# Optimization experiments

Measured on AMD Instinct MI355X. Metric: run time of the kernel, lower is better.

Reference implementation:

```python
import jax, jax.numpy as jnp
import numpy as np

H = 16           # attn_num
ROPE_THETA = 10000.0

def _rope(x):
    # x: [B, H, S, A]; non-interleaved (rotate-half) RoPE matching RotaryEmb
    A = x.shape[-1]
    S = x.shape[2]
    inv_freq = (1.0 / ROPE_THETA) ** (jnp.arange(0, A, 2, dtype=jnp.float32) / A)  # [A/2]
    t = jnp.arange(S, dtype=jnp.float32)
    freqs = t[:, None] * inv_freq[None, :]            # [S, A/2]
    cos = jnp.cos(freqs)[None, None, :, :]
    sin = jnp.sin(freqs)[None, None, :, :]
    x1, x2 = jnp.split(x, 2, axis=-1)
    y1 = x1 * cos + x2 * sin
    y2 = -x1 * sin + x2 * cos
    return jnp.concatenate([y1, y2], axis=-1).astype(x.dtype)

def setup_inputs() -> dict:
    key = jax.random.key(0)
    kq, kk, kv = jax.random.split(key, 3)
    B, S, D = 2, 2048, 2048
    return {
        "xq": jax.random.normal(kq, (B, S, D), dtype=jnp.float32),
        "xk": jax.random.normal(kk, (B, S, D), dtype=jnp.float32),
        "xv": jax.random.normal(kv, (B, S, D), dtype=jnp.float32),
    }

def reference(xq, xk, xv):
    B, S, D = xq.shape
    A = D // H
    # b s (h a) -> b h s a
    q = xq.reshape(B, S, H, A).transpose(0, 2, 1, 3)
    k = xk.reshape(B, S, H, A).transpose(0, 2, 1, 3)
    v = xv.reshape(B, S, H, A).transpose(0, 2, 1, 3)
    q = _rope(q)
    k = _rope(k)
    scale = 1.0 / jnp.sqrt(jnp.asarray(A, dtype=q.dtype))
    scores = jnp.einsum('bhsa,bhta->bhst', q, k) * scale   # [B,H,S,S]
    causal = jnp.tril(jnp.ones((S, S), dtype=bool))
    scores = jnp.where(causal[None, None, :, :], scores, jnp.asarray(-jnp.inf, scores.dtype))
    probs = jax.nn.softmax(scores, axis=-1)
    out = jnp.einsum('bhst,bhta->bhsa', probs, v)          # [B,H,S,A]
    # b h s a -> b s (h a)
    return out.transpose(0, 2, 1, 3).reshape(B, S, D)
```

## Files before the change

### kernel.cpp

```cpp
#include <hip/hip_runtime.h>
#include <stdint.h>

#define H_HEADS 16
#define ADIM    128
#define SLEN    2048
#define DMODEL  2048

typedef __attribute__((ext_vector_type(8))) short  short8;
typedef __attribute__((ext_vector_type(4))) float  float4v;
typedef __attribute__((ext_vector_type(4))) unsigned short ushort4v;

typedef const __attribute__((address_space(1))) unsigned int gas_u32;
typedef __attribute__((address_space(3))) unsigned int las_u32;

union F4 { float4 v; float a[4]; };
union PU { unsigned u[4]; short8 s; };

__device__ __forceinline__ unsigned short f2bf(float f) {
  union { float f; unsigned u; } v; v.f = f;
  unsigned r = v.u + 0x7FFFu + ((v.u >> 16) & 1u);
  return (unsigned short)(r >> 16);
}

__device__ __forceinline__ unsigned cvt_pk_bf16(float lo, float hi) {
  unsigned r;
  asm("v_cvt_pk_bf16_f32 %0, %1, %2" : "=v"(r) : "v"(lo), "v"(hi));
  return r;
}

__device__ __forceinline__ void xswap(unsigned& a, unsigned& b) {
  asm volatile("v_permlane32_swap_b32 %0, %1" : "+v"(a), "+v"(b));
  asm volatile("v_permlane16_swap_b32 %0, %1" : "+v"(a), "+v"(b));
}

__device__ __forceinline__ float fsin01(float r) { float o; asm("v_sin_f32 %0, %1" : "=v"(o) : "v"(r)); return o; }
__device__ __forceinline__ float fcos01(float r) { float o; asm("v_cos_f32 %0, %1" : "=v"(o) : "v"(r)); return o; }
__device__ __forceinline__ float ffract(float x) { float o; asm("v_fract_f32 %0, %1" : "=v"(o) : "v"(x)); return o; }
__device__ __forceinline__ float hexp2(float x)  { float o; asm("v_exp_f32 %0, %1" : "=v"(o) : "v"(x)); return o; }

#define ROPE_C 0.20762050593045935f
#define L2I2PI -2.651496129472319f
#define C2LOG  0.12751879523103988f
#define Z0     8.0f

__global__ __launch_bounds__(256) void prep_k(const float* __restrict__ xk,
                                              unsigned short* __restrict__ kw) {
  int t = blockIdx.x * 256 + threadIdx.x;
  int i4 = t & 15;
  int h  = (t >> 4) & (H_HEADS - 1);
  int s  = (t >> 8) & (SLEN - 1);
  int b  = t >> 19;
  int i0 = i4 * 4;
  long ib = ((long)(b * SLEN + s)) * DMODEL + h * ADIM;
  F4 x1, x2;
  x1.v = *(const float4*)(xk + ib + i0);
  x2.v = *(const float4*)(xk + ib + i0 + 64);
  ushort4v o1, o2;
  #pragma unroll
  for (int j = 0; j < 4; ++j) {
    float rev = (float)s * exp2f(fmaf(-(float)(i0 + j), ROPE_C, L2I2PI));
    float r = ffract(rev);
    float sn = fsin01(r), cs = fcos01(r);
    o1[j] = f2bf( x1.a[j] * cs + x2.a[j] * sn);
    o2[j] = f2bf(-x1.a[j] * sn + x2.a[j] * cs);
  }
  long row = ((long)((b * H_HEADS + h) * SLEN + s)) * ADIM;
  int swz = s & 7;
  int c1 = ((((i0     ) >> 3) ^ swz) << 3) | (i0 & 7);
  int c2 = ((((i0 + 64) >> 3) ^ swz) << 3) | (i0 & 7);
  *(ushort4v*)(kw + row + c1) = o1;
  *(ushort4v*)(kw + row + c2) = o2;
}

__global__ __launch_bounds__(256) void prep_v(const float* __restrict__ xv,
                                              unsigned short* __restrict__ vw) {
  __shared__ float lv[64 * 129];
  int jt = blockIdx.x;
  int bh = blockIdx.y;
  int b = bh >> 4, h = bh & (H_HEADS - 1);
  int t = threadIdx.x;
  #pragma unroll
  for (int it = 0; it < 8; ++it) {
    int id  = it * 256 + t;
    int row = id >> 5;
    int c4  = (id & 31) * 4;
    F4 x;
    x.v = *(const float4*)(xv + ((long)(b * SLEN + jt * 64 + row)) * DMODEL + h * ADIM + c4);
    #pragma unroll
    for (int j = 0; j < 4; ++j) lv[row * 129 + c4 + j] = x.a[j];
  }
  __syncthreads();
  int l = t & 63, w = t >> 6;
  unsigned short* vt = vw + ((long)(bh * 32 + jt)) * 8192;
  #pragma unroll
  for (int it = 0; it < 8; ++it) {
    int d = it * 16 + w * 4 + (l >> 4);
    int i = l & 15;
    ushort4v o;
    #pragma unroll
    for (int j = 0; j < 4; ++j) o[j] = f2bf(lv[(4 * i + j) * 129 + d]);
    int off = d * 64 + ((((i >> 1) ^ (d & 7)) << 3) | ((i & 1) << 2));
    *(ushort4v*)(vt + off) = o;
  }
}

__global__ __launch_bounds__(512, 1) void attn_fwd(const float* __restrict__ xq,
                                                   const unsigned short* __restrict__ kw,
                                                   const unsigned short* __restrict__ vw,
                                                   float* __restrict__ out) {
  __shared__ __align__(16) unsigned short kL[2][2][64 * 128];
  __shared__ __align__(16) unsigned short vL[2][2][128 * 64];

  int n = blockIdx.x;
  int xcd = n & 7;
  int j   = (n < 256) ? (n >> 3) : ((n - 256) >> 3);
  int bh  = xcd * 4 + (j & 3);
  int c   = (n < 256) ? (15 - (j >> 2)) : (7 - (j >> 2));
  int b = bh >> 4, h = bh & (H_HEADS - 1);
  int t = threadIdx.x, l = t & 63, w = t >> 6;
  int g = w >> 2, ww = w & 3;
  int lq = l & 15, gq = l >> 4, lq7 = lq & 7;
  int basew = c * 128 + ww * 32;
  int sq0 = basew + lq, sq1 = basew + 16 + lq;

  short8 qf0[4], qf1[4];
  auto ROPEQ = [&](int sq, short8 (&qf)[4]) {
    const float* qsrc = xq + ((long)(b * SLEN + sq)) * DMODEL + h * ADIM;
    float q32[4][8];
    #pragma unroll
    for (int cc = 0; cc < 4; ++cc) {
      F4 lo, hi;
      lo.v = *(const float4*)(qsrc + cc * 32 + gq * 8);
      hi.v = *(const float4*)(qsrc + cc * 32 + gq * 8 + 4);
      #pragma unroll
      for (int jj = 0; jj < 4; ++jj) { q32[cc][jj] = lo.a[jj]; q32[cc][jj + 4] = hi.a[jj]; }
    }
    #pragma unroll
    for (int cc = 0; cc < 2; ++cc) {
      #pragma unroll
      for (int jj = 0; jj < 8; ++jj) {
        int a = cc * 32 + gq * 8 + jj;
        float rev = (float)sq * exp2f(fmaf(-(float)a, ROPE_C, L2I2PI));
        float r = ffract(rev);
        float sn = fsin01(r), cs = fcos01(r);
        qf[cc    ][jj] = (short)f2bf( q32[cc][jj] * cs + q32[cc + 2][jj] * sn);
        qf[cc + 2][jj] = (short)f2bf(-q32[cc][jj] * sn + q32[cc + 2][jj] * cs);
      }
    }
  };
  ROPEQ(sq0, qf0);
  ROPEQ(sq1, qf1);

  float4v acc0[8], acc1[8], lacc0, lacc1;
  #pragma unroll
  for (int i = 0; i < 8; ++i) { acc0[i] = (float4v){0.f,0.f,0.f,0.f}; acc1[i] = (float4v){0.f,0.f,0.f,0.f}; }
  lacc0 = (float4v){0.f,0.f,0.f,0.f};
  lacc1 = (float4v){0.f,0.f,0.f,0.f};
  const float4v Z4 = (float4v){0.f,0.f,0.f,0.f};

  PU ones;
  ones.u[0] = 0x3F803F80u; ones.u[1] = 0x3F803F80u; ones.u[2] = 0x3F803F80u; ones.u[3] = 0x3F803F80u;

  const unsigned short* kbase_g = kw + (long)bh * SLEN * ADIM;
  const unsigned short* vbase_g = vw + (long)bh * 32 * 8192;

  const unsigned short* klr[2] = { &kL[g][0][lq * 128], &kL[g][1][lq * 128] };
  const unsigned short* vlr[2] = { &vL[g][0][lq * 64],  &vL[g][1][lq * 64]  };
  unsigned short* kst[2] = { &kL[g][0][0], &kL[g][1][0] };
  unsigned short* vst[2] = { &vL[g][0][0], &vL[g][1][0] };
  int koff[4], choff[2];
  #pragma unroll
  for (int cc = 0; cc < 4; ++cc) koff[cc] = ((cc * 4 + gq) ^ lq7) << 3;
  #pragma unroll
  for (int kc = 0; kc < 2; ++kc) choff[kc] = ((kc * 4 + gq) ^ lq7) << 3;

  auto STAGE = [&](unsigned short* kd, unsigned short* vd, int tile) {
    const unsigned short* ks = kbase_g + (long)tile * (64 * ADIM);
    const unsigned short* vs = vbase_g + (long)tile * 8192;
    #pragma unroll
    for (int sg = 0; sg < 4; ++sg) {
      int seg = ww * 4 + sg;
      __builtin_amdgcn_global_load_lds((gas_u32*)(ks + seg * 512 + l * 8),
                                       (las_u32*)&kd[seg * 512], 16, 0, 0);
      __builtin_amdgcn_global_load_lds((gas_u32*)(vs + seg * 512 + l * 8),
                                       (las_u32*)&vd[seg * 512], 16, 0, 0);
    }
  };

  auto SMAX = [&](float4v (&sv)[4], int sq, bool diag, int tj, float4v& lac, short8 (&pa)[2]) {
    float p[16];
    #pragma unroll
    for (int kb = 0; kb < 4; ++kb) {
      #pragma unroll
      for (int r = 0; r < 4; ++r) {
        float e = fmaf(sv[kb][r], C2LOG, -Z0);
        if (diag && (tj * 64 + kb * 16 + gq * 4 + r > sq)) e = -1e30f;
        p[kb * 4 + r] = hexp2(e);
      }
    }
    unsigned L[4], Hh[4];
    #pragma unroll
    for (int kb = 0; kb < 4; ++kb) {
      L[kb]  = cvt_pk_bf16(p[kb * 4 + 0], p[kb * 4 + 1]);
      Hh[kb] = cvt_pk_bf16(p[kb * 4 + 2], p[kb * 4 + 3]);
    }
    xswap(L[0], L[1]);  xswap(Hh[0], Hh[1]);
    xswap(L[2], L[3]);  xswap(Hh[2], Hh[3]);
    PU a0, a1;
    a0.u[0] = L[0]; a0.u[1] = Hh[0]; a0.u[2] = L[1]; a0.u[3] = Hh[1];
    a1.u[0] = L[2]; a1.u[1] = Hh[2]; a1.u[2] = L[3]; a1.u[3] = Hh[3];
    pa[0] = a0.s; pa[1] = a1.s;
    lac = __builtin_amdgcn_mfma_f32_16x16x32_bf16(pa[0], ones.s, lac, 0, 0, 0);
    lac = __builtin_amdgcn_mfma_f32_16x16x32_bf16(pa[1], ones.s, lac, 0, 0, 0);
  };

  int M = c + 1;

  auto ITER = [&](int m, const unsigned short* klrow, const unsigned short* vlrow,
                  unsigned short* kstN, unsigned short* vstN) {
    if (m + 1 < M) STAGE(kstN, vstN, 2 * (m + 1) + g);
    int tj = 2 * m + g;

    float4v s0[4], s1[4];
    __builtin_amdgcn_s_setprio(1);
    {
      #pragma unroll
      for (int kb = 0; kb < 4; ++kb) {
        short8 kf = *(const short8*)&klrow[kb * 2048 + koff[0]];
        s0[kb] = __builtin_amdgcn_mfma_f32_16x16x32_bf16(kf, qf0[0], Z4, 0, 0, 0);
        s1[kb] = __builtin_amdgcn_mfma_f32_16x16x32_bf16(kf, qf1[0], Z4, 0, 0, 0);
      }
      #pragma unroll
      for (int cc = 1; cc < 4; ++cc) {
        #pragma unroll
        for (int kb = 0; kb < 4; ++kb) {
          short8 kf = *(const short8*)&klrow[kb * 2048 + koff[cc]];
          s0[kb] = __builtin_amdgcn_mfma_f32_16x16x32_bf16(kf, qf0[cc], s0[kb], 0, 0, 0);
          s1[kb] = __builtin_amdgcn_mfma_f32_16x16x32_bf16(kf, qf1[cc], s1[kb], 0, 0, 0);
        }
      }
    }
    __builtin_amdgcn_s_setprio(0);

    bool diag = (m == M - 1);
    short8 pa0[2], pa1[2];
    SMAX(s0, sq0, diag, tj, lacc0, pa0);
    SMAX(s1, sq1, diag, tj, lacc1, pa1);

    __builtin_amdgcn_s_setprio(1);
    #pragma unroll
    for (int kc = 0; kc < 2; ++kc) {
      #pragma unroll
      for (int db = 0; db < 8; ++db) {
        short8 vb = *(const short8*)&vlrow[db * 1024 + choff[kc]];
        acc0[db] = __builtin_amdgcn_mfma_f32_16x16x32_bf16(pa0[kc], vb, acc0[db], 0, 0, 0);
        acc1[db] = __builtin_amdgcn_mfma_f32_16x16x32_bf16(pa1[kc], vb, acc1[db], 0, 0, 0);
      }
    }
    __builtin_amdgcn_s_setprio(0);

    asm volatile("s_waitcnt vmcnt(0)" ::: "memory");
    __builtin_amdgcn_s_barrier();
  };

  STAGE(kst[0], vst[0], g);
  asm volatile("s_waitcnt vmcnt(0)" ::: "memory");
  __builtin_amdgcn_s_barrier();

  int m = 0;
  for (; m + 2 <= M; m += 2) {
    ITER(m,     klr[0], vlr[0], kst[1], vst[1]);
    ITER(m + 1, klr[1], vlr[1], kst[0], vst[0]);
  }
  if (m < M) ITER(m, klr[0], vlr[0], kst[1], vst[1]);

  float4v* mergeO = (float4v*)&kL[0][0][0];
  float4v* mergeL = (float4v*)&vL[0][0][0];
  if (g == 1) {
    float4v* dst = mergeO + ww * 1024;
    #pragma unroll
    for (int i = 0; i < 8; ++i) {
      dst[i * 64 + l]       = acc0[i];
      dst[(8 + i) * 64 + l] = acc1[i];
    }
    float4v* ld = mergeL + ww * 128;
    ld[l]      = lacc0;
    ld[64 + l] = lacc1;
  }
  __builtin_amdgcn_s_barrier();

  if (g == 0) {
    const float4v* src = mergeO + ww * 1024;
    #pragma unroll
    for (int i = 0; i < 8; ++i) {
      float4v b0 = src[i * 64 + l];
      float4v b1 = src[(8 + i) * 64 + l];
      #pragma unroll
      for (int r = 0; r < 4; ++r) { acc0[i][r] += b0[r]; acc1[i][r] += b1[r]; }
    }
    const float4v* ls = mergeL + ww * 128;
    float4v lb0 = ls[l], lb1 = ls[64 + l];
    #pragma unroll
    for (int r = 0; r < 4; ++r) { lacc0[r] += lb0[r]; lacc1[r] += lb1[r]; }

    auto EPI = [&](int base, float4v& lac, float4v (&acc)[8]) {
      float linv[4];
      #pragma unroll
      for (int r = 0; r < 4; ++r) linv[r] = 1.0f / lac[r];
      #pragma unroll
      for (int db = 0; db < 8; ++db)
        #pragma unroll
        for (int r = 0; r < 4; ++r)
          out[((long)(b * SLEN + base + gq * 4 + r)) * DMODEL + h * ADIM + db * 16 + lq]
            = acc[db][r] * linv[r];
    };
    EPI(basew,      lacc0, acc0);
    EPI(basew + 16, lacc1, acc1);
  }
}

extern "C" void kernel_launch(void* const* d_in, const int* in_sizes, int n_in,
                              void* d_out, int out_size, void* d_ws, size_t ws_size,
                              hipStream_t stream) {
  const float* xq = (const float*)d_in[0];
  const float* xk = (const float*)d_in[1];
  const float* xv = (const float*)d_in[2];
  float* outp = (float*)d_out;
  int B = in_sizes[0] / (SLEN * DMODEL);
  size_t perT = (size_t)B * H_HEADS * SLEN * ADIM;
  unsigned short* kw = (unsigned short*)d_ws;
  unsigned short* vw = kw + perT;

  prep_k<<<dim3(B * 2048), 256, 0, stream>>>(xk, kw);
  prep_v<<<dim3(32, B * H_HEADS), 256, 0, stream>>>(xv, vw);
  attn_fwd<<<dim3(B * H_HEADS * 16), 512, 0, stream>>>(xq, kw, vw, outp);
}
```

Baseline: 76.08 us.

## Shrink attention tiles to 64 query rows and 16-key steps with 256-thread blocks

The attention kernel moves from 512-thread blocks handling 128 query rows with 64-key tiles to 256-thread blocks handling 64 query rows with 16-key tiles, doubling the grid and targeting three blocks per CU. The V prep kernel is rewritten to emit a 16-key-granular transposed layout that matches the new tile shape, and the causal diagonal mask is computed per tile. The aim is better occupancy and finer causal trimming with less LDS per block. The cost is a 16-key step per iteration, which means more barriers and prefetch stages per unit of work and less MFMA work between synchronisations.

```diff
diff --git a/kernel.cpp b/kernel.cpp
--- a/kernel.cpp
+++ b/kernel.cpp
@@ -9,6 +9,7 @@
 typedef __attribute__((ext_vector_type(8))) short  short8;
 typedef __attribute__((ext_vector_type(4))) float  float4v;
 typedef __attribute__((ext_vector_type(4))) unsigned short ushort4v;
+typedef __attribute__((ext_vector_type(8))) unsigned short ushort8v;
 
 typedef const __attribute__((address_space(1))) unsigned int gas_u32;
 typedef __attribute__((address_space(3))) unsigned int las_u32;
@@ -21,18 +22,15 @@
   unsigned r = v.u + 0x7FFFu + ((v.u >> 16) & 1u);
   return (unsigned short)(r >> 16);
 }
-
 __device__ __forceinline__ unsigned cvt_pk_bf16(float lo, float hi) {
   unsigned r;
   asm("v_cvt_pk_bf16_f32 %0, %1, %2" : "=v"(r) : "v"(lo), "v"(hi));
   return r;
 }
-
 __device__ __forceinline__ void xswap(unsigned& a, unsigned& b) {
   asm volatile("v_permlane32_swap_b32 %0, %1" : "+v"(a), "+v"(b));
   asm volatile("v_permlane16_swap_b32 %0, %1" : "+v"(a), "+v"(b));
 }
-
 __device__ __forceinline__ float fsin01(float r) { float o; asm("v_sin_f32 %0, %1" : "=v"(o) : "v"(r)); return o; }
 __device__ __forceinline__ float fcos01(float r) { float o; asm("v_cos_f32 %0, %1" : "=v"(o) : "v"(r)); return o; }
 __device__ __forceinline__ float ffract(float x) { float o; asm("v_fract_f32 %0, %1" : "=v"(o) : "v"(x)); return o; }
@@ -74,53 +72,48 @@
 
 __global__ __launch_bounds__(256) void prep_v(const float* __restrict__ xv,
                                               unsigned short* __restrict__ vw) {
-  __shared__ float lv[64 * 129];
+  __shared__ float lv[16 * 129];
   int jt = blockIdx.x;
   int bh = blockIdx.y;
   int b = bh >> 4, h = bh & (H_HEADS - 1);
   int t = threadIdx.x;
   #pragma unroll
-  for (int it = 0; it < 8; ++it) {
+  for (int it = 0; it < 2; ++it) {
     int id  = it * 256 + t;
     int row = id >> 5;
     int c4  = (id & 31) * 4;
     F4 x;
-    x.v = *(const float4*)(xv + ((long)(b * SLEN + jt * 64 + row)) * DMODEL + h * ADIM + c4);
-    #pragma unroll
-    for (int j = 0; j < 4; ++j) lv[row * 129 + c4 + j] = x.a[j];
+    x.v = *(const float4*)(xv + ((long)(b * SLEN + jt * 16 + row)) * DMODEL + h * ADIM + c4);
+    #pragma unroll
+    for (int jj = 0; jj < 4; ++jj) lv[row * 129 + c4 + jj] = x.a[jj];
   }
   __syncthreads();
-  int l = t & 63, w = t >> 6;
-  unsigned short* vt = vw + ((long)(bh * 32 + jt)) * 8192;
-  #pragma unroll
-  for (int it = 0; it < 8; ++it) {
-    int d = it * 16 + w * 4 + (l >> 4);
-    int i = l & 15;
-    ushort4v o;
-    #pragma unroll
-    for (int j = 0; j < 4; ++j) o[j] = f2bf(lv[(4 * i + j) * 129 + d]);
-    int off = d * 64 + ((((i >> 1) ^ (d & 7)) << 3) | ((i & 1) << 2));
-    *(ushort4v*)(vt + off) = o;
-  }
-}
-
-__global__ __launch_bounds__(512, 1) void attn_fwd(const float* __restrict__ xq,
+  int d = t >> 1, half = t & 1;
+  ushort8v o;
+  #pragma unroll
+  for (int jj = 0; jj < 8; ++jj) o[jj] = f2bf(lv[(half * 8 + jj) * 129 + d]);
+  *(ushort8v*)(vw + ((long)(bh * 128 + jt)) * 2048 + d * 16 + half * 8) = o;
+}
+
+__global__ __launch_bounds__(256, 3) void attn_fwd(const float* __restrict__ xq,
                                                    const unsigned short* __restrict__ kw,
                                                    const unsigned short* __restrict__ vw,
                                                    float* __restrict__ out) {
-  __shared__ __align__(16) unsigned short kL[2][2][64 * 128];
-  __shared__ __align__(16) unsigned short vL[2][2][128 * 64];
+  __shared__ __align__(16) unsigned char sbuf[36864];
+  unsigned short* kB = (unsigned short*)sbuf;
+  unsigned short* vB = (unsigned short*)(sbuf + 16384);
+  float4v* mergeO = (float4v*)sbuf;
+  float4v* mergeL = (float4v*)(sbuf + 32768);
 
   int n = blockIdx.x;
-  int xcd = n & 7;
-  int j   = (n < 256) ? (n >> 3) : ((n - 256) >> 3);
-  int bh  = xcd * 4 + (j & 3);
-  int c   = (n < 256) ? (15 - (j >> 2)) : (7 - (j >> 2));
+  int xcd = n & 7, j = n >> 3;
+  int bh = xcd * 4 + (j & 3);
+  int c  = 31 - (j >> 2);
   int b = bh >> 4, h = bh & (H_HEADS - 1);
   int t = threadIdx.x, l = t & 63, w = t >> 6;
-  int g = w >> 2, ww = w & 3;
+  int wq = w >> 1, g = w & 1;
   int lq = l & 15, gq = l >> 4, lq7 = lq & 7;
-  int basew = c * 128 + ww * 32;
+  int basew = c * 64 + wq * 32;
   int sq0 = basew + lq, sq1 = basew + 16 + lq;
 
   short8 qf0[4], qf1[4];
@@ -161,25 +154,24 @@
   PU ones;
   ones.u[0] = 0x3F803F80u; ones.u[1] = 0x3F803F80u; ones.u[2] = 0x3F803F80u; ones.u[3] = 0x3F803F80u;
 
-  const unsigned short* kbase_g = kw + (long)bh * SLEN * ADIM;
-  const unsigned short* vbase_g = vw + (long)bh * 32 * 8192;
-
-  const unsigned short* klr[2] = { &kL[g][0][lq * 128], &kL[g][1][lq * 128] };
-  const unsigned short* vlr[2] = { &vL[g][0][lq * 64],  &vL[g][1][lq * 64]  };
-  unsigned short* kst[2] = { &kL[g][0][0], &kL[g][1][0] };
-  unsigned short* vst[2] = { &vL[g][0][0], &vL[g][1][0] };
-  int koff[4], choff[2];
+  const unsigned short* kbase = kw + (long)bh * SLEN * ADIM;
+  const unsigned short* vbase = vw + (long)bh * 128 * 2048;
+
+  unsigned short* kst[2] = { kB + (g * 2 + 0) * 2048, kB + (g * 2 + 1) * 2048 };
+  unsigned short* vst[2] = { vB + (g * 2 + 0) * 2048, vB + (g * 2 + 1) * 2048 };
+  const unsigned short* klr[2] = { kst[0] + lq * 128, kst[1] + lq * 128 };
+  const unsigned short* vlr[2] = { vst[0] + lq * 16 + (gq & 1) * 8,
+                                   vst[1] + lq * 16 + (gq & 1) * 8 };
+  int koff[4];
   #pragma unroll
   for (int cc = 0; cc < 4; ++cc) koff[cc] = ((cc * 4 + gq) ^ lq7) << 3;
-  #pragma unroll
-  for (int kc = 0; kc < 2; ++kc) choff[kc] = ((kc * 4 + gq) ^ lq7) << 3;
 
   auto STAGE = [&](unsigned short* kd, unsigned short* vd, int tile) {
-    const unsigned short* ks = kbase_g + (long)tile * (64 * ADIM);
-    const unsigned short* vs = vbase_g + (long)tile * 8192;
-    #pragma unroll
-    for (int sg = 0; sg < 4; ++sg) {
-      int seg = ww * 4 + sg;
+    const unsigned short* ks = kbase + (long)tile * 2048;
+    const unsigned short* vs = vbase + (long)tile * 2048;
+    #pragma unroll
+    for (int i = 0; i < 2; ++i) {
+      int seg = wq * 2 + i;
       __builtin_amdgcn_global_load_lds((gas_u32*)(ks + seg * 512 + l * 8),
                                        (las_u32*)&kd[seg * 512], 16, 0, 0);
       __builtin_amdgcn_global_load_lds((gas_u32*)(vs + seg * 512 + l * 8),
@@ -187,75 +179,57 @@
     }
   };
 
-  auto SMAX = [&](float4v (&sv)[4], int sq, bool diag, int tj, float4v& lac, short8 (&pa)[2]) {
-    float p[16];
-    #pragma unroll
-    for (int kb = 0; kb < 4; ++kb) {
-      #pragma unroll
-      for (int r = 0; r < 4; ++r) {
-        float e = fmaf(sv[kb][r], C2LOG, -Z0);
-        if (diag && (tj * 64 + kb * 16 + gq * 4 + r > sq)) e = -1e30f;
-        p[kb * 4 + r] = hexp2(e);
-      }
-    }
-    unsigned L[4], Hh[4];
-    #pragma unroll
-    for (int kb = 0; kb < 4; ++kb) {
-      L[kb]  = cvt_pk_bf16(p[kb * 4 + 0], p[kb * 4 + 1]);
-      Hh[kb] = cvt_pk_bf16(p[kb * 4 + 2], p[kb * 4 + 3]);
-    }
-    xswap(L[0], L[1]);  xswap(Hh[0], Hh[1]);
-    xswap(L[2], L[3]);  xswap(Hh[2], Hh[3]);
-    PU a0, a1;
-    a0.u[0] = L[0]; a0.u[1] = Hh[0]; a0.u[2] = L[1]; a0.u[3] = Hh[1];
-    a1.u[0] = L[2]; a1.u[1] = Hh[2]; a1.u[2] = L[3]; a1.u[3] = Hh[3];
-    pa[0] = a0.s; pa[1] = a1.s;
-    lac = __builtin_amdgcn_mfma_f32_16x16x32_bf16(pa[0], ones.s, lac, 0, 0, 0);
-    lac = __builtin_amdgcn_mfma_f32_16x16x32_bf16(pa[1], ones.s, lac, 0, 0, 0);
+  auto SMAX = [&](float4v sv, int sq, bool dg, int tj, float4v& lac) -> short8 {
+    float p[4];
+    #pragma unroll
+    for (int r = 0; r < 4; ++r) {
+      float e = fmaf(sv[r], C2LOG, -Z0);
+      if (dg && (tj * 16 + gq * 4 + r > sq)) e = -1e30f;
+      p[r] = hexp2(e);
+    }
+    unsigned L0 = cvt_pk_bf16(p[0], p[1]);
+    unsigned H0 = cvt_pk_bf16(p[2], p[3]);
+    unsigned L1 = 0u, H1 = 0u;
+    xswap(L0, L1);
+    xswap(H0, H1);
+    PU a;
+    a.u[0] = L0; a.u[1] = H0; a.u[2] = L1; a.u[3] = H1;
+    lac = __builtin_amdgcn_mfma_f32_16x16x32_bf16(a.s, ones.s, lac, 0, 0, 0);
+    return a.s;
   };
 
-  int M = c + 1;
+  int M = 2 * c + 2;
 
   auto ITER = [&](int m, const unsigned short* klrow, const unsigned short* vlrow,
-                  unsigned short* kstN, unsigned short* vstN) {
-    if (m + 1 < M) STAGE(kstN, vstN, 2 * (m + 1) + g);
+                  unsigned short* kn, unsigned short* vn) {
+    if (m + 1 < M) STAGE(kn, vn, 2 * (m + 1) + g);
     int tj = 2 * m + g;
 
-    float4v s0[4], s1[4];
+    float4v s0, s1;
     __builtin_amdgcn_s_setprio(1);
     {
-      #pragma unroll
-      for (int kb = 0; kb < 4; ++kb) {
-        short8 kf = *(const short8*)&klrow[kb * 2048 + koff[0]];
-        s0[kb] = __builtin_amdgcn_mfma_f32_16x16x32_bf16(kf, qf0[0], Z4, 0, 0, 0);
-        s1[kb] = __builtin_amdgcn_mfma_f32_16x16x32_bf16(kf, qf1[0], Z4, 0, 0, 0);
+      short8 kf = *(const short8*)&klrow[koff[0]];
+      s0 = __builtin_amdgcn_mfma_f32_16x16x32_bf16(kf, qf0[0], Z4, 0, 0, 0);
+      s1 = __builtin_amdgcn_mfma_f32_16x16x32_bf16(kf, qf1[0], Z4, 0, 0, 0);
+      #pragma unroll
+      for (int cc = 1; cc < 4; ++cc) {
+        kf = *(const short8*)&klrow[koff[cc]];
+        s0 = __builtin_amdgcn_mfma_f32_16x16x32_bf16(kf, qf0[cc], s0, 0, 0, 0);
+        s1 = __builtin_amdgcn_mfma_f32_16x16x32_bf16(kf, qf1[cc], s1, 0, 0, 0);
       }
-      #pragma unroll
-      for (int cc = 1; cc < 4; ++cc) {
-        #pragma unroll
-        for (int kb = 0; kb < 4; ++kb) {
-          short8 kf = *(const short8*)&klrow[kb * 2048 + koff[cc]];
-          s0[kb] = __builtin_amdgcn_mfma_f32_16x16x32_bf16(kf, qf0[cc], s0[kb], 0, 0, 0);
-          s1[kb] = __builtin_amdgcn_mfma_f32_16x16x32_bf16(kf, qf1[cc], s1[kb], 0, 0, 0);
-        }
-      }
     }
     __builtin_amdgcn_s_setprio(0);
 
-    bool diag = (m == M - 1);
-    short8 pa0[2], pa1[2];
-    SMAX(s0, sq0, diag, tj, lacc0, pa0);
-    SMAX(s1, sq1, diag, tj, lacc1, pa1);
+    bool dg = (tj * 16 + 15 > basew);
+    short8 pa0 = SMAX(s0, sq0, dg, tj, lacc0);
+    short8 pa1 = SMAX(s1, sq1, dg, tj, lacc1);
 
     __builtin_amdgcn_s_setprio(1);
     #pragma unroll
-    for (int kc = 0; kc < 2; ++kc) {
-      #pragma unroll
-      for (int db = 0; db < 8; ++db) {
-        short8 vb = *(const short8*)&vlrow[db * 1024 + choff[kc]];
-        acc0[db] = __builtin_amdgcn_mfma_f32_16x16x32_bf16(pa0[kc], vb, acc0[db], 0, 0, 0);
-        acc1[db] = __builtin_amdgcn_mfma_f32_16x16x32_bf16(pa1[kc], vb, acc1[db], 0, 0, 0);
-      }
+    for (int db = 0; db < 8; ++db) {
+      short8 vb = *(const short8*)&vlrow[db * 256];
+      acc0[db] = __builtin_amdgcn_mfma_f32_16x16x32_bf16(pa0, vb, acc0[db], 0, 0, 0);
+      acc1[db] = __builtin_amdgcn_mfma_f32_16x16x32_bf16(pa1, vb, acc1[db], 0, 0, 0);
     }
     __builtin_amdgcn_s_setprio(0);
 
@@ -267,30 +241,26 @@
   asm volatile("s_waitcnt vmcnt(0)" ::: "memory");
   __builtin_amdgcn_s_barrier();
 
-  int m = 0;
-  for (; m + 2 <= M; m += 2) {
+  for (int m = 0; m < M; m += 2) {
     ITER(m,     klr[0], vlr[0], kst[1], vst[1]);
     ITER(m + 1, klr[1], vlr[1], kst[0], vst[0]);
   }
-  if (m < M) ITER(m, klr[0], vlr[0], kst[1], vst[1]);
-
-  float4v* mergeO = (float4v*)&kL[0][0][0];
-  float4v* mergeL = (float4v*)&vL[0][0][0];
+
   if (g == 1) {
-    float4v* dst = mergeO + ww * 1024;
+    float4v* dst = mergeO + wq * 1024;
     #pragma unroll
     for (int i = 0; i < 8; ++i) {
       dst[i * 64 + l]       = acc0[i];
       dst[(8 + i) * 64 + l] = acc1[i];
     }
-    float4v* ld = mergeL + ww * 128;
+    float4v* ld = mergeL + wq * 128;
     ld[l]      = lacc0;
     ld[64 + l] = lacc1;
   }
   __builtin_amdgcn_s_barrier();
 
   if (g == 0) {
-    const float4v* src = mergeO + ww * 1024;
+    const float4v* src = mergeO + wq * 1024;
     #pragma unroll
     for (int i = 0; i < 8; ++i) {
       float4v b0 = src[i * 64 + l];
@@ -298,7 +268,7 @@
       #pragma unroll
       for (int r = 0; r < 4; ++r) { acc0[i][r] += b0[r]; acc1[i][r] += b1[r]; }
     }
-    const float4v* ls = mergeL + ww * 128;
+    const float4v* ls = mergeL + wq * 128;
     float4v lb0 = ls[l], lb1 = ls[64 + l];
     #pragma unroll
     for (int r = 0; r < 4; ++r) { lacc0[r] += lb0[r]; lacc1[r] += lb1[r]; }
@@ -332,6 +302,6 @@
   unsigned short* vw = kw + perT;
 
   prep_k<<<dim3(B * 2048), 256, 0, stream>>>(xk, kw);
-  prep_v<<<dim3(32, B * H_HEADS), 256, 0, stream>>>(xv, vw);
-  attn_fwd<<<dim3(B * H_HEADS * 16), 512, 0, stream>>>(xq, kw, vw, outp);
-}
+  prep_v<<<dim3(128, B * H_HEADS), 256, 0, stream>>>(xv, vw);
+  attn_fwd<<<dim3(B * H_HEADS * 32), 256, 0, stream>>>(xq, kw, vw, outp);
+}
```

Result: slower. 81.83 us (+7.6%).

## Software-pipeline QK of next tile with softmax and PV of current tile

Applied to the files above, without the earlier changes.

Restructures the attention main loop so the QK^T MFMAs for tile m+1 are issued before the softmax and PV of tile m. K staging is moved one tile further ahead of V staging. This lets exp/convert VALU work overlap with matrix-core work and breaks the serial QK→softmax→PV dependency within each iteration. In exchange it needs more live score registers (two sets of score accumulators), which may raise VGPR pressure or lower occupancy. The loop-tail handling also becomes more intricate.

```diff
diff --git a/kernel.cpp b/kernel.cpp
--- a/kernel.cpp
+++ b/kernel.cpp
@@ -21,18 +21,15 @@
   unsigned r = v.u + 0x7FFFu + ((v.u >> 16) & 1u);
   return (unsigned short)(r >> 16);
 }
-
 __device__ __forceinline__ unsigned cvt_pk_bf16(float lo, float hi) {
   unsigned r;
   asm("v_cvt_pk_bf16_f32 %0, %1, %2" : "=v"(r) : "v"(lo), "v"(hi));
   return r;
 }
-
 __device__ __forceinline__ void xswap(unsigned& a, unsigned& b) {
   asm volatile("v_permlane32_swap_b32 %0, %1" : "+v"(a), "+v"(b));
   asm volatile("v_permlane16_swap_b32 %0, %1" : "+v"(a), "+v"(b));
 }
-
 __device__ __forceinline__ float fsin01(float r) { float o; asm("v_sin_f32 %0, %1" : "=v"(o) : "v"(r)); return o; }
 __device__ __forceinline__ float fcos01(float r) { float o; asm("v_cos_f32 %0, %1" : "=v"(o) : "v"(r)); return o; }
 __device__ __forceinline__ float ffract(float x) { float o; asm("v_fract_f32 %0, %1" : "=v"(o) : "v"(x)); return o; }
@@ -174,17 +171,43 @@
   #pragma unroll
   for (int kc = 0; kc < 2; ++kc) choff[kc] = ((kc * 4 + gq) ^ lq7) << 3;
 
-  auto STAGE = [&](unsigned short* kd, unsigned short* vd, int tile) {
+  auto STAGE_K = [&](unsigned short* kd, int tile) {
     const unsigned short* ks = kbase_g + (long)tile * (64 * ADIM);
-    const unsigned short* vs = vbase_g + (long)tile * 8192;
     #pragma unroll
     for (int sg = 0; sg < 4; ++sg) {
       int seg = ww * 4 + sg;
       __builtin_amdgcn_global_load_lds((gas_u32*)(ks + seg * 512 + l * 8),
                                        (las_u32*)&kd[seg * 512], 16, 0, 0);
+    }
+  };
+  auto STAGE_V = [&](unsigned short* vd, int tile) {
+    const unsigned short* vs = vbase_g + (long)tile * 8192;
+    #pragma unroll
+    for (int sg = 0; sg < 4; ++sg) {
+      int seg = ww * 4 + sg;
       __builtin_amdgcn_global_load_lds((gas_u32*)(vs + seg * 512 + l * 8),
                                        (las_u32*)&vd[seg * 512], 16, 0, 0);
     }
+  };
+
+  auto QK = [&](const unsigned short* klrow, float4v (&sA)[4], float4v (&sB)[4]) {
+    __builtin_amdgcn_s_setprio(1);
+    #pragma unroll
+    for (int kb = 0; kb < 4; ++kb) {
+      short8 kf = *(const short8*)&klrow[kb * 2048 + koff[0]];
+      sA[kb] = __builtin_amdgcn_mfma_f32_16x16x32_bf16(kf, qf0[0], Z4, 0, 0, 0);
+      sB[kb] = __builtin_amdgcn_mfma_f32_16x16x32_bf16(kf, qf1[0], Z4, 0, 0, 0);
+    }
+    #pragma unroll
+    for (int cc = 1; cc < 4; ++cc) {
+      #pragma unroll
+      for (int kb = 0; kb < 4; ++kb) {
+        short8 kf = *(const short8*)&klrow[kb * 2048 + koff[cc]];
+        sA[kb] = __builtin_amdgcn_mfma_f32_16x16x32_bf16(kf, qf0[cc], sA[kb], 0, 0, 0);
+        sB[kb] = __builtin_amdgcn_mfma_f32_16x16x32_bf16(kf, qf1[cc], sB[kb], 0, 0, 0);
+      }
+    }
+    __builtin_amdgcn_s_setprio(0);
   };
 
   auto SMAX = [&](float4v (&sv)[4], int sq, bool diag, int tj, float4v& lac, short8 (&pa)[2]) {
@@ -214,39 +237,7 @@
     lac = __builtin_amdgcn_mfma_f32_16x16x32_bf16(pa[1], ones.s, lac, 0, 0, 0);
   };
 
-  int M = c + 1;
-
-  auto ITER = [&](int m, const unsigned short* klrow, const unsigned short* vlrow,
-                  unsigned short* kstN, unsigned short* vstN) {
-    if (m + 1 < M) STAGE(kstN, vstN, 2 * (m + 1) + g);
-    int tj = 2 * m + g;
-
-    float4v s0[4], s1[4];
-    __builtin_amdgcn_s_setprio(1);
-    {
-      #pragma unroll
-      for (int kb = 0; kb < 4; ++kb) {
-        short8 kf = *(const short8*)&klrow[kb * 2048 + koff[0]];
-        s0[kb] = __builtin_amdgcn_mfma_f32_16x16x32_bf16(kf, qf0[0], Z4, 0, 0, 0);
-        s1[kb] = __builtin_amdgcn_mfma_f32_16x16x32_bf16(kf, qf1[0], Z4, 0, 0, 0);
-      }
-      #pragma unroll
-      for (int cc = 1; cc < 4; ++cc) {
-        #pragma unroll
-        for (int kb = 0; kb < 4; ++kb) {
-          short8 kf = *(const short8*)&klrow[kb * 2048 + koff[cc]];
-          s0[kb] = __builtin_amdgcn_mfma_f32_16x16x32_bf16(kf, qf0[cc], s0[kb], 0, 0, 0);
-          s1[kb] = __builtin_amdgcn_mfma_f32_16x16x32_bf16(kf, qf1[cc], s1[kb], 0, 0, 0);
-        }
-      }
-    }
-    __builtin_amdgcn_s_setprio(0);
-
-    bool diag = (m == M - 1);
-    short8 pa0[2], pa1[2];
-    SMAX(s0, sq0, diag, tj, lacc0, pa0);
-    SMAX(s1, sq1, diag, tj, lacc1, pa1);
-
+  auto PVf = [&](const unsigned short* vlrow, short8 (&pa0)[2], short8 (&pa1)[2]) {
     __builtin_amdgcn_s_setprio(1);
     #pragma unroll
     for (int kc = 0; kc < 2; ++kc) {
@@ -258,21 +249,48 @@
       }
     }
     __builtin_amdgcn_s_setprio(0);
-
+  };
+
+  int M = c + 1;
+  float4v sE0[4], sE1[4], sO0[4], sO1[4];
+  short8 pa0[2], pa1[2];
+
+  STAGE_K(kst[0], g);
+  STAGE_V(vst[0], g);
+  if (M > 1) STAGE_K(kst[1], 2 + g);
+  asm volatile("s_waitcnt vmcnt(0)" ::: "memory");
+  __builtin_amdgcn_s_barrier();
+  QK(klr[0], sE0, sE1);
+
+  int m = 0;
+  for (; m + 2 <= M; m += 2) {
+    if (m + 2 < M) STAGE_K(kst[0], 2 * (m + 2) + g);
+    STAGE_V(vst[1], 2 * (m + 1) + g);
+    QK(klr[1], sO0, sO1);
+    SMAX(sE0, sq0, false, 2 * m + g, lacc0, pa0);
+    SMAX(sE1, sq1, false, 2 * m + g, lacc1, pa1);
+    PVf(vlr[0], pa0, pa1);
     asm volatile("s_waitcnt vmcnt(0)" ::: "memory");
     __builtin_amdgcn_s_barrier();
-  };
-
-  STAGE(kst[0], vst[0], g);
-  asm volatile("s_waitcnt vmcnt(0)" ::: "memory");
-  __builtin_amdgcn_s_barrier();
-
-  int m = 0;
-  for (; m + 2 <= M; m += 2) {
-    ITER(m,     klr[0], vlr[0], kst[1], vst[1]);
-    ITER(m + 1, klr[1], vlr[1], kst[0], vst[0]);
-  }
-  if (m < M) ITER(m, klr[0], vlr[0], kst[1], vst[1]);
+
+    if (m + 3 < M) STAGE_K(kst[1], 2 * (m + 3) + g);
+    if (m + 2 < M) STAGE_V(vst[0], 2 * (m + 2) + g);
+    if (m + 2 < M) QK(klr[0], sE0, sE1);
+    {
+      bool dg = (m + 1 == M - 1);
+      SMAX(sO0, sq0, dg, 2 * (m + 1) + g, lacc0, pa0);
+      SMAX(sO1, sq1, dg, 2 * (m + 1) + g, lacc1, pa1);
+    }
+    PVf(vlr[1], pa0, pa1);
+    asm volatile("s_waitcnt vmcnt(0)" ::: "memory");
+    __builtin_amdgcn_s_barrier();
+  }
+  if (m < M) {
+    SMAX(sE0, sq0, true, 2 * m + g, lacc0, pa0);
+    SMAX(sE1, sq1, true, 2 * m + g, lacc1, pa1);
+    PVf(vlr[0], pa0, pa1);
+    __builtin_amdgcn_s_barrier();
+  }
 
   float4v* mergeO = (float4v*)&kL[0][0][0];
   float4v* mergeL = (float4v*)&vL[0][0][0];
```

After: 77.01 us. About the same (+1.2%).
